# Kernel tuning notes

Hardware: AMD Instinct MI355X
Metric: run time of the kernel (lower is better)

## Reference

```python
import jax, jax.numpy as jnp
import numpy as np
import math

B, S, D, L = 16, 512, 512, 5
H = 1
DK = D // H
FF = 2 * D
VOCAB = 30
REL_VOCAB = 301  # max_relative_1d_positions + 1
SPAN = 10        # attention_span_list[0]; loop index bug keeps it fixed for all layers
EPS = 1e-5


def setup_inputs() -> dict:
    key = jax.random.key(0)
    ks = jax.random.split(key, 20)
    s = 0.02
    inp = {
        "x": jax.random.randint(ks[0], (B, S), 0, VOCAB, dtype=jnp.int64),
        "tok_emb": jax.random.normal(ks[1], (VOCAB, D), jnp.float32) * s,
        "rel_emb": jax.random.normal(ks[2], (REL_VOCAB, D), jnp.float32) * s,
        "Wq": jax.random.normal(ks[3], (L, D, D), jnp.float32) * s,
        "bq": jnp.zeros((L, D), jnp.float32),
        "Wk": jax.random.normal(ks[4], (L, D, D), jnp.float32) * s,
        "bk": jnp.zeros((L, D), jnp.float32),
        "Wv": jax.random.normal(ks[5], (L, D, D), jnp.float32) * s,
        "bv": jnp.zeros((L, D), jnp.float32),
        "Wo": jax.random.normal(ks[6], (L, D, D), jnp.float32) * s,
        "bo": jnp.zeros((L, D), jnp.float32),
        "W1": jax.random.normal(ks[7], (L, D, FF), jnp.float32) * s,
        "b1": jnp.zeros((L, FF), jnp.float32),
        "W2": jax.random.normal(ks[8], (L, FF, D), jnp.float32) * s,
        "b2": jnp.zeros((L, D), jnp.float32),
        "ln1_g": jnp.ones((L, D), jnp.float32),
        "ln1_b": jnp.zeros((L, D), jnp.float32),
        "ln2_g": jnp.ones((L, D), jnp.float32),
        "ln2_b": jnp.zeros((L, D), jnp.float32),
    }
    return inp


def _layernorm(h, g, b):
    mu = jnp.mean(h, axis=-1, keepdims=True)
    var = jnp.mean((h - mu) ** 2, axis=-1, keepdims=True)
    return (h - mu) * jax.lax.rsqrt(var + EPS) * g + b


def reference(x, tok_emb, rel_emb, Wq, bq, Wk, bk, Wv, bv, Wo, bo,
              W1, b1, W2, b2, ln1_g, ln1_b, ln2_g, ln2_b):
    seq_len = x.shape[1]
    scale = 1.0 / math.sqrt(DK)

    # relative-position bias matrix, shared by all layers (span bug in original)
    r = jnp.arange(seq_len)
    dist = jnp.clip(jnp.abs(r[None, :] - r[:, None]), 0, SPAN)  # [S,S]
    rel = rel_emb[dist]  # [S,S,D]

    causal = jnp.tril(jnp.ones((seq_len, seq_len), dtype=bool))  # [S,S]

    h = tok_emb[x]  # [B,S,D]
    for l in range(L):
        q = h @ Wq[l] + bq[l]  # [B,S,D]
        k = h @ Wk[l] + bk[l]
        v = h @ Wv[l] + bv[l]
        # heads=1: [B,S,D] acts as [B,H=1,S,DK]
        score1 = jnp.einsum('bid,bjd->bij', q, k) * scale
        score2 = jnp.einsum('bid,ijd->bij', q, rel)
        # NOTE: original divides (score1 + score2) by sqrt(d_k) again
        scores = (score1 + score2) * scale
        scores = jnp.where(causal[None, :, :], scores, -1e9)
        p = jax.nn.softmax(scores, axis=-1)
        ctx = jnp.einsum('bij,bjd->bid', p, v)
        x_att = ctx @ Wo[l] + bo[l]
        h = _layernorm(h + x_att, ln1_g[l], ln1_b[l])
        ff = jax.nn.relu(h @ W1[l] + b1[l]) @ W2[l] + b2[l]
        h = _layernorm(h + ff, ln2_g[l], ln2_b[l])
    return h
```

## Files before the change

### kernel.cpp

```cpp
#include <hip/hip_runtime.h>
#include <math.h>

#define S 512
#define D 512
#define FFD 1024
#define NB 16
#define NL 5

typedef __attribute__((ext_vector_type(8))) short bf16x8;
typedef __attribute__((ext_vector_type(4))) float f32x4;

__device__ __forceinline__ short f2bf(float f){
  union { float f; unsigned u; } c; c.f = f;
  unsigned r = c.u + 0x7FFFu + ((c.u >> 16) & 1u);
  return (short)(r >> 16);
}
__device__ __forceinline__ float bf2f(short s){
  union { unsigned u; float f; } c; c.u = ((unsigned)(unsigned short)s) << 16;
  return c.f;
}

__device__ __forceinline__ void gload16(const void* g, void* l){
  __builtin_amdgcn_global_load_lds(
      (const __attribute__((address_space(1))) void*)g,
      (__attribute__((address_space(3))) void*)l, 16, 0, 0);
}

__device__ __forceinline__ float wsum(float v){
  #pragma unroll
  for (int o = 32; o; o >>= 1) v += __shfl_down(v, o, 64);
  return v;
}
__device__ __forceinline__ float bsum(float v, float* s){
  v = wsum(v);
  __syncthreads();
  if ((threadIdx.x & 63) == 0) s[threadIdx.x >> 6] = v;
  __syncthreads();
  return s[0] + s[1] + s[2] + s[3];
}

__global__ __launch_bounds__(256) void embed_k(const int* __restrict__ x,
    const float* __restrict__ tok, short* __restrict__ hb){
  int idx = blockIdx.x * 256 + threadIdx.x;
  int row = idx >> 9;
  int d   = idx & 511;
  hb[idx] = f2bf(tok[x[row] * D + d]);
}

__global__ __launch_bounds__(256) void bcat_k(const float* __restrict__ bq,
    const float* __restrict__ bk, const float* __restrict__ bv,
    const float* __restrict__ rel, float* __restrict__ out){
  int i = blockIdx.x * 256 + threadIdx.x;
  if (i >= NL * 1664) return;
  int lay = i / 1664, c = i % 1664;
  float v;
  if      (c <  512) v = bq[lay * 512 + c];
  else if (c < 1024) v = bk[lay * 512 + c - 512];
  else if (c < 1536) v = bv[lay * 512 + c - 1024];
  else if (c < 1547){
    int cc = c - 1536;
    float s = 0.f;
    for (int j = 0; j < 512; j++) s += bq[lay * 512 + j] * rel[cc * 512 + j];
    v = s;
  } else v = 0.f;
  out[i] = v;
}

__global__ __launch_bounds__(256) void wrel_k(
    const float* __restrict__ Wq, const float* __restrict__ rel,
    short* __restrict__ WqkvT){
  const int bid = blockIdx.x;
  const int lay = bid >> 7, kc = bid & 127;
  const int w = threadIdx.x >> 6, lane = threadIdx.x & 63;
  const int k = kc * 4 + w;
  const float* wrow = Wq + (size_t)lay * 262144 + (size_t)k * 512 + lane * 8;
  float qv[8];
  #pragma unroll
  for (int e = 0; e < 8; e++) qv[e] = wrow[e];
  short* dst = WqkvT + (size_t)lay * 851968;
  #pragma unroll
  for (int c = 0; c < 11; c++){
    const float* rp = rel + c * 512 + lane * 8;
    float s = 0.f;
    #pragma unroll
    for (int e = 0; e < 8; e++) s = fmaf(qv[e], rp[e], s);
    s = wsum(s);
    if (lane == 0) dst[(size_t)(1536 + c) * 512 + k] = f2bf(s);
  }
  if (lane == 0){
    #pragma unroll
    for (int c = 11; c < 16; c++) dst[(size_t)(1536 + c) * 512 + k] = 0;
  }
}

__global__ __launch_bounds__(256) void wtrans_k(
    const float* __restrict__ Wq, const float* __restrict__ Wk,
    const float* __restrict__ Wv, const float* __restrict__ Wo,
    const float* __restrict__ W1, const float* __restrict__ W2,
    short* __restrict__ WqkvT, short* __restrict__ WoT,
    short* __restrict__ W1T, short* __restrict__ W2T)
{
  __shared__ float tl[64][65];
  int id = blockIdx.x;
  const float* src; short* dst; int K, N, tk, tn;
  if (id < 1280){
    int mat = id / 320, r = id % 320, lay = r / 64, tt = r % 64;
    tk = tt >> 3; tn = tt & 7; K = 512; N = 512;
    const float* s;
    short* d;
    if (mat == 0){ s = Wq; d = WqkvT + (size_t)lay * 851968; }
    else if (mat == 1){ s = Wk; d = WqkvT + (size_t)lay * 851968 + 262144; }
    else if (mat == 2){ s = Wv; d = WqkvT + (size_t)lay * 851968 + 524288; }
    else { s = Wo; d = WoT + (size_t)lay * 262144; }
    src = s + (size_t)lay * 262144; dst = d;
  } else if (id < 1920){
    int r = id - 1280, lay = r / 128, tt = r % 128;
    tk = tt >> 4; tn = tt & 15; K = 512; N = 1024;
    src = W1 + (size_t)lay * 524288; dst = W1T + (size_t)lay * 524288;
  } else {
    int r = id - 1920, lay = r / 128, tt = r % 128;
    tk = tt >> 3; tn = tt & 7; K = 1024; N = 512;
    src = W2 + (size_t)lay * 524288; dst = W2T + (size_t)lay * 524288;
  }
  const int k0 = tk * 64, n0 = tn * 64;
  const int t = threadIdx.x;
  const int lr = t >> 4, lc = (t & 15) * 4;
  #pragma unroll
  for (int s = 0; s < 4; s++){
    int row = lr + s * 16;
    float4 v = *(const float4*)&src[(size_t)(k0 + row) * N + n0 + lc];
    tl[row][lc + 0] = v.x; tl[row][lc + 1] = v.y;
    tl[row][lc + 2] = v.z; tl[row][lc + 3] = v.w;
  }
  __syncthreads();
  const int nr8 = t >> 3, kc8 = (t & 7) * 8;
  #pragma unroll
  for (int s = 0; s < 2; s++){
    int nr = nr8 + s * 32;
    bf16x8 o;
    #pragma unroll
    for (int e = 0; e < 8; e++) o[e] = f2bf(tl[kc8 + e][nr]);
    *(bf16x8*)&dst[(size_t)(n0 + nr) * K + k0 + kc8] = o;
  }
}

template<int ROWS, int PAN>
__device__ __forceinline__ void stage_tile(const short* __restrict__ G, int ld,
                                           int kbase, char* ldsBase, int w, int l){
  constexpr int CALLS = ROWS * PAN / 64;
  #pragma unroll
  for (int c = 0; c < CALLS; c++){
    const int idx = w * CALLS + c;
    const int panel = idx / (ROWS / 16);
    const int chunk = idx % (ROWS / 16);
    const short* src = G + (size_t)(chunk * 16 + (l >> 2)) * ld
                         + kbase + panel * 32 + (l & 3) * 8;
    gload16(src, ldsBase + idx * 1024);
  }
}

template<int BM, int BN, int MODE, int BK>
__global__ __launch_bounds__(256) void mm_nt(
    const short* __restrict__ A, int ldA,
    const short* __restrict__ B, int ldB,
    const float* __restrict__ bias, void* __restrict__ C, int ldC,
    const float* __restrict__ qrel, short* __restrict__ vT,
    float* __restrict__ qrelOut,
    int K, long batA, long batB, long batC)
{
  constexpr int PAN = BK / 32;
  constexpr int STAGE_SH = 2 * BK * (BM + BN);
  constexpr int BOUNCE_SH = BM * BN;
  constexpr int SMEM_SH = STAGE_SH > BOUNCE_SH ? STAGE_SH : BOUNCE_SH;
  __shared__ short smem[SMEM_SH];
  short* As = smem;
  short* Bs = smem + 2 * BM * BK;

  const int gx = gridDim.x, gy = gridDim.y;
  int flat = ((int)blockIdx.z * gy + (int)blockIdx.y) * gx + (int)blockIdx.x;
  const int nwg = gx * gy * (int)gridDim.z;
  const int chunk = nwg >> 3;
  flat = (flat & 7) * chunk + (flat >> 3);
  const int bx = flat % gx;
  const int byy = (flat / gx) % gy;
  const int b = flat / (gx * gy);

  const int m0 = byy * BM, n0 = bx * BN;
  if (MODE == 3 && n0 > m0) return;
  int nk = K / BK;
  if (MODE == 4){ int km = (m0 + BM) / BK; nk = km < nk ? km : nk; }

  constexpr int FM = BM / 32, FN = BN / 32;
  f32x4 acc[FM][FN];
  const f32x4 z = {0.f, 0.f, 0.f, 0.f};
  #pragma unroll
  for (int m = 0; m < FM; m++)
    #pragma unroll
    for (int n = 0; n < FN; n++) acc[m][n] = z;

  const int t = threadIdx.x, l = t & 63, w = t >> 6;
  const short* Ag = A + (size_t)b * batA + (size_t)m0 * ldA;
  const short* Bg = B + (size_t)b * batB + (size_t)n0 * ldB;

  stage_tile<BM, PAN>(Ag, ldA, 0, (char*)As, w, l);
  stage_tile<BN, PAN>(Bg, ldB, 0, (char*)Bs, w, l);
  __syncthreads();

  const int wm = (w >> 1) * (BM / 2), wn = (w & 1) * (BN / 2);
  const int kc = (l >> 4) * 8;
  float rs[FM];
  #pragma unroll
  for (int m = 0; m < FM; m++) rs[m] = 0.f;

  for (int ks = 0; ks < nk; ks++){
    const int cur = ks & 1;
    if (ks + 1 < nk){
      const int nxt = cur ^ 1;
      stage_tile<BM, PAN>(Ag, ldA, (ks + 1) * BK, (char*)As + nxt * (BM * BK * 2), w, l);
      stage_tile<BN, PAN>(Bg, ldB, (ks + 1) * BK, (char*)Bs + nxt * (BN * BK * 2), w, l);
    }
    const short* Ab = As + cur * (BM * BK);
    const short* Bb = Bs + cur * (BN * BK);
    #pragma unroll
    for (int p = 0; p < PAN; p++){
      bf16x8 af[FM], bfr[FN];
      #pragma unroll
      for (int m = 0; m < FM; m++)
        af[m] = *(const bf16x8*)&Ab[p * BM * 32 + (wm + m * 16 + (l & 15)) * 32 + kc];
      #pragma unroll
      for (int n = 0; n < FN; n++)
        bfr[n] = *(const bf16x8*)&Bb[p * BN * 32 + (wn + n * 16 + (l & 15)) * 32 + kc];
      if (MODE == 4){
        #pragma unroll
        for (int m = 0; m < FM; m++){
          float s = 0.f;
          #pragma unroll
          for (int e = 0; e < 8; e++) s += bf2f(af[m][e]);
          rs[m] += s;
        }
      }
      #pragma unroll
      for (int m = 0; m < FM; m++)
        #pragma unroll
        for (int n = 0; n < FN; n++)
          acc[m][n] = __builtin_amdgcn_mfma_f32_16x16x32_bf16(af[m], bfr[n], acc[m][n], 0, 0, 0);
    }
    __syncthreads();
  }

  float invr[FM][4];
  if (MODE == 4){
    #pragma unroll
    for (int m = 0; m < FM; m++){
      float r = rs[m];
      r += __shfl_xor(r, 16, 64);
      r += __shfl_xor(r, 32, 64);
      #pragma unroll
      for (int rr = 0; rr < 4; rr++)
        invr[m][rr] = 1.0f / __shfl(r, (l >> 4) * 4 + rr, 64);
    }
  }

  const size_t cbase = (size_t)b * batC;

  if (MODE == 5 && n0 >= 1024){
    if (n0 < 1536){
      #pragma unroll
      for (int m = 0; m < FM; m++){
        const int rbase = m0 + wm + m * 16 + (l >> 4) * 4;
        #pragma unroll
        for (int n = 0; n < FN; n++){
          const int col = n0 + wn + n * 16 + (l & 15);
          const int d = col - 1024;
          const int bb = rbase >> 9, s0 = rbase & 511;
          union { short s[4]; uint2 u; } tmp;
          #pragma unroll
          for (int r = 0; r < 4; r++) tmp.s[r] = f2bf(acc[m][n][r] + bias[col]);
          *(uint2*)&vT[(size_t)bb * 262144 + (size_t)d * 512 + s0] = tmp.u;
        }
      }
    } else {
      #pragma unroll
      for (int m = 0; m < FM; m++){
        const int rbase = m0 + wm + m * 16 + (l >> 4) * 4;
        #pragma unroll
        for (int n = 0; n < FN; n++){
          const int col = n0 + wn + n * 16 + (l & 15);
          if (col < 1552){
            const int c = col - 1536;
            #pragma unroll
            for (int r = 0; r < 4; r++)
              qrelOut[(size_t)(rbase + r) * 16 + c] = acc[m][n][r] + bias[col];
          }
        }
      }
    }
    return;
  }

  #pragma unroll
  for (int m = 0; m < FM; m++){
    const int rb = wm + m * 16 + (l >> 4) * 4;
    #pragma unroll
    for (int n = 0; n < FN; n++){
      const int cl = wn + n * 16 + (l & 15);
      const int col = n0 + cl;
      #pragma unroll
      for (int r = 0; r < 4; r++){
        const int row = m0 + rb + r;
        float v = acc[m][n][r];
        short ov;
        if (MODE == 3){
          if (col <= row){
            int dd = row - col; if (dd > 10) dd = 10;
            float sv = v * (1.0f / 512.0f)
                     + qrel[((size_t)b * S + row) * 16 + dd] * 0.044194173824159216f;
            ov = f2bf(__expf(sv));
          } else ov = 0;
        } else if (MODE == 4){
          ov = f2bf(v * invr[m][r]);
        } else {
          v += bias[col];
          if (MODE == 2) v = fmaxf(v, 0.f);
          ov = f2bf(v);
        }
        smem[(rb + r) * BN + cl] = ov;
      }
    }
  }
  __syncthreads();
  constexpr int ITER = BM * BN / 2048;
  #pragma unroll
  for (int c = 0; c < ITER; c++){
    const int idx = c * 2048 + t * 8;
    const int row = idx / BN, cc = idx % BN;
    *(bf16x8*)&((short*)C)[cbase + (size_t)(m0 + row) * ldC + n0 + cc] =
        *(const bf16x8*)&smem[idx];
  }
}

template<int FINAL>
__global__ __launch_bounds__(256) void add_ln_k(
    short* __restrict__ hb, const short* __restrict__ y,
    const float* __restrict__ g, const float* __restrict__ be,
    float* __restrict__ hOut)
{
  __shared__ float red[4];
  const int row = blockIdx.x;
  short* hbr = hb + (size_t)row * D;
  const short* yr = y + (size_t)row * D;
  const int t = threadIdx.x;
  float v0 = bf2f(hbr[t])       + bf2f(yr[t]);
  float v1 = bf2f(hbr[t + 256]) + bf2f(yr[t + 256]);
  float mu = bsum(v0 + v1, red) * (1.0f / 512.0f);
  float d0 = v0 - mu, d1 = v1 - mu;
  float var = bsum(d0 * d0 + d1 * d1, red) * (1.0f / 512.0f);
  float rcp = rsqrtf(var + 1e-5f);
  float o0 = d0 * rcp * g[t]       + be[t];
  float o1 = d1 * rcp * g[t + 256] + be[t + 256];
  if (FINAL){
    float* ho = hOut + (size_t)row * D;
    ho[t]       = o0;
    ho[t + 256] = o1;
  } else {
    hbr[t]       = f2bf(o0);
    hbr[t + 256] = f2bf(o1);
  }
}

extern "C" void kernel_launch(void* const* d_in, const int* in_sizes, int n_in,
                              void* d_out, int out_size, void* d_ws, size_t ws_size,
                              hipStream_t stream)
{
  const int*   x   = (const int*)  d_in[0];
  const float* tok = (const float*)d_in[1];
  const float* rel = (const float*)d_in[2];
  const float* Wq  = (const float*)d_in[3];  const float* bq = (const float*)d_in[4];
  const float* Wk  = (const float*)d_in[5];  const float* bk = (const float*)d_in[6];
  const float* Wv  = (const float*)d_in[7];  const float* bv = (const float*)d_in[8];
  const float* Wo  = (const float*)d_in[9];  const float* bo = (const float*)d_in[10];
  const float* W1  = (const float*)d_in[11]; const float* b1 = (const float*)d_in[12];
  const float* W2  = (const float*)d_in[13]; const float* b2 = (const float*)d_in[14];
  const float* g1  = (const float*)d_in[15]; const float* be1 = (const float*)d_in[16];
  const float* g2  = (const float*)d_in[17]; const float* be2 = (const float*)d_in[18];
  (void)in_sizes; (void)n_in; (void)out_size; (void)ws_size;

  float* h = (float*)d_out;

  char* ws = (char*)d_ws;
  const size_t MB = 1 << 20;
  short* hb     = (short*)(ws);
  short* qkv    = (short*)(ws + 8 * MB);
  short* vT     = (short*)(ws + 24 * MB);
  short* p      = (short*)(ws + 32 * MB);
  short* ctx    = (short*)(ws + 40 * MB);
  short* xatt   = (short*)(ws + 48 * MB);
  short* ffmid  = (short*)(ws + 32 * MB);
  float* qrelb  = (float*)(ws + 56 * MB);
  float* bqkv   = (float*)(ws + 56 * MB + 512 * 1024);
  short* wb     = (short*)(ws + 57 * MB);
  short* WqkvT  = wb;
  short* WoT    = WqkvT + (size_t)5 * 851968;
  short* W1T    = WoT   + (size_t)5 * 262144;
  short* W2T    = W1T   + (size_t)5 * 524288;
  short* ffout  = xatt;

  const int M = NB * S;

  wtrans_k<<<2560, 256, 0, stream>>>(Wq, Wk, Wv, Wo, W1, W2, WqkvT, WoT, W1T, W2T);
  wrel_k<<<640, 256, 0, stream>>>(Wq, rel, WqkvT);
  bcat_k<<<(NL * 1664 + 255) / 256, 256, 0, stream>>>(bq, bk, bv, rel, bqkv);
  embed_k<<<(size_t)M * D / 256, 256, 0, stream>>>(x, tok, hb);

  for (int l = 0; l < NL; l++){
    mm_nt<128, 128, 5, 32><<<dim3(13, 64, 1), 256, 0, stream>>>(
        hb, 512, WqkvT + (size_t)l * 851968, 512, bqkv + l * 1664,
        qkv, 1024, nullptr, vT, qrelb, 512, 0, 0, 0);

    mm_nt<64, 64, 3, 64><<<dim3(8, 8, NB), 256, 0, stream>>>(
        qkv, 1024, qkv + 512, 1024, nullptr,
        p, 512, qrelb, nullptr, nullptr, 512,
        (long)S * 1024, (long)S * 1024, (long)S * S);

    mm_nt<64, 64, 4, 64><<<dim3(8, 8, NB), 256, 0, stream>>>(
        p, 512, vT, 512, nullptr,
        ctx, 512, nullptr, nullptr, nullptr, 512,
        (long)S * S, (long)D * S, (long)S * D);

    mm_nt<128, 64, 1, 64><<<dim3(8, 64, 1), 256, 0, stream>>>(
        ctx, 512, WoT + (size_t)l * 262144, 512, bo + l * 512,
        xatt, 512, nullptr, nullptr, nullptr, 512, 0, 0, 0);
    add_ln_k<0><<<M, 256, 0, stream>>>(hb, xatt, g1 + l * 512, be1 + l * 512, nullptr);

    mm_nt<128, 128, 2, 32><<<dim3(8, 64, 1), 256, 0, stream>>>(
        hb, 512, W1T + (size_t)l * 524288, 512, b1 + l * 1024,
        ffmid, 1024, nullptr, nullptr, nullptr, 512, 0, 0, 0);
    mm_nt<128, 64, 1, 64><<<dim3(8, 64, 1), 256, 0, stream>>>(
        ffmid, 1024, W2T + (size_t)l * 524288, 1024, b2 + l * 512,
        ffout, 512, nullptr, nullptr, nullptr, 1024, 0, 0, 0);
    if (l < NL - 1)
      add_ln_k<0><<<M, 256, 0, stream>>>(hb, ffout, g2 + l * 512, be2 + l * 512, nullptr);
    else
      add_ln_k<1><<<M, 256, 0, stream>>>(hb, ffout, g2 + l * 512, be2 + l * 512, h);
  }
}
```

Measured before the change: 570.0 us.

## Stage V-transpose through LDS, use wave-per-row LayerNorm, widen attention tiles

```diff
diff --git a/kernel.cpp b/kernel.cpp
--- a/kernel.cpp
+++ b/kernel.cpp
@@ -30,13 +30,6 @@
   #pragma unroll
   for (int o = 32; o; o >>= 1) v += __shfl_down(v, o, 64);
   return v;
-}
-__device__ __forceinline__ float bsum(float v, float* s){
-  v = wsum(v);
-  __syncthreads();
-  if ((threadIdx.x & 63) == 0) s[threadIdx.x >> 6] = v;
-  __syncthreads();
-  return s[0] + s[1] + s[2] + s[3];
 }
 
 __global__ __launch_bounds__(256) void embed_k(const int* __restrict__ x,
@@ -171,7 +164,10 @@
   constexpr int PAN = BK / 32;
   constexpr int STAGE_SH = 2 * BK * (BM + BN);
   constexpr int BOUNCE_SH = BM * BN;
-  constexpr int SMEM_SH = STAGE_SH > BOUNCE_SH ? STAGE_SH : BOUNCE_SH;
+  constexpr int TB_ST = BM + 8;
+  constexpr int TBOUNCE_SH = (MODE == 5) ? BN * TB_ST : 0;
+  constexpr int SMEM_A = STAGE_SH > BOUNCE_SH ? STAGE_SH : BOUNCE_SH;
+  constexpr int SMEM_SH = SMEM_A > TBOUNCE_SH ? SMEM_A : TBOUNCE_SH;
   __shared__ short smem[SMEM_SH];
   short* As = smem;
   short* Bs = smem + 2 * BM * BK;
@@ -186,7 +182,7 @@
   const int b = flat / (gx * gy);
 
   const int m0 = byy * BM, n0 = bx * BN;
-  if (MODE == 3 && n0 > m0) return;
+  if (MODE == 3 && n0 >= m0 + BM) return;
   int nk = K / BK;
   if (MODE == 4){ int km = (m0 + BM) / BK; nk = km < nk ? km : nk; }
 
@@ -265,20 +261,33 @@
 
   if (MODE == 5 && n0 >= 1024){
     if (n0 < 1536){
+      short* tb = smem;
       #pragma unroll
       for (int m = 0; m < FM; m++){
-        const int rbase = m0 + wm + m * 16 + (l >> 4) * 4;
+        const int rb = wm + m * 16 + (l >> 4) * 4;
         #pragma unroll
         for (int n = 0; n < FN; n++){
-          const int col = n0 + wn + n * 16 + (l & 15);
-          const int d = col - 1024;
-          const int bb = rbase >> 9, s0 = rbase & 511;
+          const int cl = wn + n * 16 + (l & 15);
+          const int col = n0 + cl;
           union { short s[4]; uint2 u; } tmp;
           #pragma unroll
           for (int r = 0; r < 4; r++) tmp.s[r] = f2bf(acc[m][n][r] + bias[col]);
-          *(uint2*)&vT[(size_t)bb * 262144 + (size_t)d * 512 + s0] = tmp.u;
+          *(uint2*)&tb[cl * TB_ST + rb] = tmp.u;
         }
       }
+      __syncthreads();
+      const int dbase = n0 - 1024;
+      constexpr int ITER_T = BM * BN / 2048;
+      #pragma unroll
+      for (int c = 0; c < ITER_T; c++){
+        const int idx = c * 2048 + t * 8;
+        const int dl = idx / BM, sl = idx % BM;
+        const int grow = m0 + sl;
+        const int bb = grow >> 9, s0 = grow & 511;
+        *(bf16x8*)&vT[(size_t)bb * 262144 + (size_t)(dbase + dl) * 512 + s0] =
+            *(const bf16x8*)&tb[dl * TB_ST + sl];
+      }
+      return;
     } else {
       #pragma unroll
       for (int m = 0; m < FM; m++){
@@ -294,8 +303,8 @@
           }
         }
       }
+      return;
     }
-    return;
   }
 
   #pragma unroll
@@ -345,26 +354,45 @@
     const float* __restrict__ g, const float* __restrict__ be,
     float* __restrict__ hOut)
 {
-  __shared__ float red[4];
-  const int row = blockIdx.x;
+  const int t = threadIdx.x, w = t >> 6, l = t & 63;
+  const int row = blockIdx.x * 4 + w;
   short* hbr = hb + (size_t)row * D;
   const short* yr = y + (size_t)row * D;
-  const int t = threadIdx.x;
-  float v0 = bf2f(hbr[t])       + bf2f(yr[t]);
-  float v1 = bf2f(hbr[t + 256]) + bf2f(yr[t + 256]);
-  float mu = bsum(v0 + v1, red) * (1.0f / 512.0f);
-  float d0 = v0 - mu, d1 = v1 - mu;
-  float var = bsum(d0 * d0 + d1 * d1, red) * (1.0f / 512.0f);
-  float rcp = rsqrtf(var + 1e-5f);
-  float o0 = d0 * rcp * g[t]       + be[t];
-  float o1 = d1 * rcp * g[t + 256] + be[t + 256];
+  bf16x8 h8 = *(const bf16x8*)&hbr[l * 8];
+  bf16x8 y8 = *(const bf16x8*)&yr[l * 8];
+  float v[8], s1 = 0.f, s2 = 0.f;
+  #pragma unroll
+  for (int e = 0; e < 8; e++){
+    v[e] = bf2f(h8[e]) + bf2f(y8[e]);
+    s1 += v[e];
+    s2 += v[e] * v[e];
+  }
+  #pragma unroll
+  for (int o = 32; o; o >>= 1){
+    s1 += __shfl_xor(s1, o, 64);
+    s2 += __shfl_xor(s2, o, 64);
+  }
+  const float mu  = s1 * (1.0f / 512.0f);
+  const float var = s2 * (1.0f / 512.0f) - mu * mu;
+  const float rcp = rsqrtf(var + 1e-5f);
+  float4 g0 = *(const float4*)&g[l * 8];
+  float4 g1 = *(const float4*)&g[l * 8 + 4];
+  float4 b0 = *(const float4*)&be[l * 8];
+  float4 b1 = *(const float4*)&be[l * 8 + 4];
+  float gv[8] = {g0.x, g0.y, g0.z, g0.w, g1.x, g1.y, g1.z, g1.w};
+  float bv[8] = {b0.x, b0.y, b0.z, b0.w, b1.x, b1.y, b1.z, b1.w};
+  float o[8];
+  #pragma unroll
+  for (int e = 0; e < 8; e++) o[e] = (v[e] - mu) * rcp * gv[e] + bv[e];
   if (FINAL){
-    float* ho = hOut + (size_t)row * D;
-    ho[t]       = o0;
-    ho[t + 256] = o1;
+    float* ho = hOut + (size_t)row * D + l * 8;
+    *(float4*)&ho[0] = make_float4(o[0], o[1], o[2], o[3]);
+    *(float4*)&ho[4] = make_float4(o[4], o[5], o[6], o[7]);
   } else {
-    hbr[t]       = f2bf(o0);
-    hbr[t + 256] = f2bf(o1);
+    bf16x8 ob;
+    #pragma unroll
+    for (int e = 0; e < 8; e++) ob[e] = f2bf(o[e]);
+    *(bf16x8*)&hbr[l * 8] = ob;
   }
 }
 
@@ -417,12 +445,12 @@
         hb, 512, WqkvT + (size_t)l * 851968, 512, bqkv + l * 1664,
         qkv, 1024, nullptr, vT, qrelb, 512, 0, 0, 0);
 
-    mm_nt<64, 64, 3, 64><<<dim3(8, 8, NB), 256, 0, stream>>>(
+    mm_nt<64, 128, 3, 64><<<dim3(4, 8, NB), 256, 0, stream>>>(
         qkv, 1024, qkv + 512, 1024, nullptr,
         p, 512, qrelb, nullptr, nullptr, 512,
         (long)S * 1024, (long)S * 1024, (long)S * S);
 
-    mm_nt<64, 64, 4, 64><<<dim3(8, 8, NB), 256, 0, stream>>>(
+    mm_nt<64, 128, 4, 64><<<dim3(4, 8, NB), 256, 0, stream>>>(
         p, 512, vT, 512, nullptr,
         ctx, 512, nullptr, nullptr, nullptr, 512,
         (long)S * S, (long)D * S, (long)S * D);
@@ -430,7 +458,7 @@
     mm_nt<128, 64, 1, 64><<<dim3(8, 64, 1), 256, 0, stream>>>(
         ctx, 512, WoT + (size_t)l * 262144, 512, bo + l * 512,
         xatt, 512, nullptr, nullptr, nullptr, 512, 0, 0, 0);
-    add_ln_k<0><<<M, 256, 0, stream>>>(hb, xatt, g1 + l * 512, be1 + l * 512, nullptr);
+    add_ln_k<0><<<M / 4, 256, 0, stream>>>(hb, xatt, g1 + l * 512, be1 + l * 512, nullptr);
 
     mm_nt<128, 128, 2, 32><<<dim3(8, 64, 1), 256, 0, stream>>>(
         hb, 512, W1T + (size_t)l * 524288, 512, b1 + l * 1024,
@@ -439,8 +467,8 @@
         ffmid, 1024, W2T + (size_t)l * 524288, 1024, b2 + l * 512,
         ffout, 512, nullptr, nullptr, nullptr, 1024, 0, 0, 0);
     if (l < NL - 1)
-      add_ln_k<0><<<M, 256, 0, stream>>>(hb, ffout, g2 + l * 512, be2 + l * 512, nullptr);
+      add_ln_k<0><<<M / 4, 256, 0, stream>>>(hb, ffout, g2 + l * 512, be2 + l * 512, nullptr);
     else
-      add_ln_k<1><<<M, 256, 0, stream>>>(hb, ffout, g2 + l * 512, be2 + l * 512, h);
-  }
-}
+      add_ln_k<1><<<M / 4, 256, 0, stream>>>(hb, ffout, g2 + l * 512, be2 + l * 512, h);
+  }
+}
```

After: 538.7 us. 1.06x faster.
